# Performance work log

Measured on AMD Instinct MI355X. Metric: run time of the kernel, lower is better.

The kernel has to match this reference:

```python
import jax, jax.numpy as jnp
import numpy as np

B, L, T = 4096, 1024, 32
START, STOP = T - 2, T - 1
NEG = -10000.0


def setup_inputs() -> dict:
    key = jax.random.key(0)
    k1, k2, k3 = jax.random.split(key, 3)
    feats = jax.random.normal(k1, (B, L, T), dtype=jnp.float32)
    transitions = jax.random.normal(k2, (T, T), dtype=jnp.float32)
    # CRF structural constraints from __init__: nothing transitions TO START,
    # nothing transitions FROM STOP. transitions[next, prev] convention.
    transitions = transitions.at[START, :].set(NEG).at[:, STOP].set(NEG)
    tags = jax.random.randint(k3, (B, L), 0, T - 2, dtype=jnp.int64)
    return {"feats": feats, "transitions": transitions, "tags": tags}


def reference(feats, transitions, tags):
    # feats: [B, L, T] emissions, transitions: [T, T] (next, prev), tags: [B, L]
    b, l, t = feats.shape

    # ---- forward algorithm (log partition), scan over time ----
    init = jnp.full((b, t), NEG, dtype=feats.dtype).at[:, START].set(0.0)

    def step(fv, feat_t):  # fv: [B, T] over prev tags, feat_t: [B, T]
        # tag_var[b, next, prev] = fv[b, prev] + trans[next, prev] + emit[b, next]
        tag_var = fv[:, None, :] + transitions[None, :, :] + feat_t[:, :, None]
        return jax.nn.logsumexp(tag_var, axis=2), None

    fv, _ = jax.lax.scan(step, init, jnp.swapaxes(feats, 0, 1))  # scan over L
    alpha = jax.nn.logsumexp(fv + transitions[STOP][None, :], axis=1)  # [B]

    # ---- gold path score ----
    tags_ext = jnp.concatenate(
        [jnp.full((b, 1), START, dtype=tags.dtype), tags], axis=1
    )  # [B, L+1]
    trans_score = transitions[tags_ext[:, 1:], tags_ext[:, :-1]].sum(axis=1)
    emit_score = jnp.take_along_axis(feats, tags[:, :, None], axis=2)[:, :, 0].sum(axis=1)
    gold = trans_score + emit_score + transitions[STOP, tags[:, -1]]

    return alpha - gold  # per-sequence negative log-likelihood [B]
```

## Files before the change

### kernel.cpp

```cpp
#include <hip/hip_runtime.h>
#include <hip/hip_bf16.h>


#define BATCH 4096
#define LSEQ  1024
#define T     32
#define START 30
#define STOP  31

typedef __attribute__((ext_vector_type(8))) short short8;
typedef __attribute__((ext_vector_type(4))) float f32x4;

static __device__ __forceinline__ short bf16b(float x) {
    union { __hip_bfloat16 h; short s; } u;
    u.h = __float2bfloat16(x);
    return u.s;
}

__global__ __launch_bounds__(64) void crf_fwd_mfma(
    const float* __restrict__ feats,
    const float* __restrict__ trans,
    const int*   __restrict__ tags,
    float*       __restrict__ out)
{
    __shared__ float trans_s[T * T];
    const int lane = threadIdx.x;
    for (int i = lane; i < T * T; i += 64) trans_s[i] = trans[i];
    __syncthreads();

    const int n = lane & 15;
    const int q = lane >> 4;
    const int b = blockIdx.x * 16 + n;

    short8 a1, a2;
    {
        const int s1 = 8 * (n >> 2) + (n & 3);
        const int s2 = s1 + 4;
#pragma unroll
        for (int j = 0; j < 8; ++j) {
            a1[j] = bf16b(__expf(trans_s[s1 * T + 8 * q + j]));
            a2[j] = bf16b(__expf(trans_s[s2 * T + 8 * q + j]));
        }
    }

    short8 bfrag;
#pragma unroll
    for (int j = 0; j < 8; ++j) bfrag[j] = 0;
    if (q == 3) bfrag[6] = bf16b(1.0f);

    const f32x4* fp = (const f32x4*)(feats + (size_t)b * (LSEQ * T) + 8 * q);
    const int*   tb = tags + (size_t)b * LSEQ;

    f32x4 fr0[8], fr1[8];
    int   tbuf[8];
#pragma unroll
    for (int i = 0; i < 8; ++i) {
        fr0[i] = fp[i * 8];
        fr1[i] = fp[i * 8 + 1];
        tbuf[i] = tb[i];
    }

    float mAcc  = 0.0f;
    float mAccF = 0.0f;
    float gold_trans = 0.0f;
    float gold_emit  = 0.0f;
    int   prev_tag = START;
    float ev[8];

    const f32x4 zacc = {0.f, 0.f, 0.f, 0.f};

#define CRF_STEP(l, slot, DO_PF)                                               \
    {                                                                          \
        const f32x4 f0  = fr0[slot];                                           \
        const f32x4 f1  = fr1[slot];                                           \
        const int   tag = tbuf[slot];                                          \
        if (DO_PF) {                                                           \
            fr0[slot]  = fp[((l) + 8) * 8];                                    \
            fr1[slot]  = fp[((l) + 8) * 8 + 1];                                \
            tbuf[slot] = tb[(l) + 8];                                          \
        }                                                                      \
                      \
        const float f00 = __shfl(f0[0], n, 64);                                \
        float e0[4], e1[4];                                                    \
        _Pragma("unroll")                                                      \
        for (int r = 0; r < 4; ++r) {                                          \
            e0[r] = __expf(f0[r] - f00);                                       \
            e1[r] = __expf(f1[r] - f00);                                       \
        }                                                                      \
        f32x4 c1 = __builtin_amdgcn_mfma_f32_16x16x32_bf16(a1, bfrag, zacc, 0, 0, 0); \
        f32x4 c2 = __builtin_amdgcn_mfma_f32_16x16x32_bf16(a2, bfrag, zacc, 0, 0, 0); \
                             \
        const float cb  = __shfl(c1[0], n, 64);   \
        const float inv = __builtin_amdgcn_rcpf(cb);                           \
        mAcc  += __logf(cb);            \
        mAccF += f00;                                                          \
        _Pragma("unroll")                                                      \
        for (int r = 0; r < 4; ++r) {                                          \
            ev[r]     = (c1[r] * e0[r]) * inv;                                 \
            ev[4 + r] = (c2[r] * e1[r]) * inv;                                 \
        }                                                                      \
        _Pragma("unroll")                                                      \
        for (int j = 0; j < 8; ++j) bfrag[j] = bf16b(ev[j]);                   \
         \
        gold_trans += trans_s[tag * T + prev_tag];                             \
        {                                                                      \
            const f32x4 fs  = (tag & 4) ? f1 : f0;                             \
            const float p01 = (tag & 1) ? fs[1] : fs[0];                       \
            const float p23 = (tag & 1) ? fs[3] : fs[2];                       \
            const float pk  = (tag & 2) ? p23 : p01;                           \
            if ((tag >> 3) == q) gold_emit += pk;                              \
        }                                                                      \
        prev_tag = tag;                                                        \
    }

    for (int lo = 0; lo < LSEQ - 8; lo += 8) {
#pragma unroll
        for (int i = 0; i < 8; ++i) CRF_STEP(lo + i, i, 1)
    }
#pragma unroll
    for (int i = 0; i < 8; ++i) CRF_STEP(LSEQ - 8 + i, i, 0)
#undef CRF_STEP

    float s = 0.0f;
#pragma unroll
    for (int j = 0; j < 8; ++j)
        s += ev[j] * __expf(trans_s[STOP * T + 8 * q + j]);
    s += __shfl_xor(s, 16, 64);
    s += __shfl_xor(s, 32, 64);
    const float alpha = mAcc + mAccF + __logf(s);

    float ge = gold_emit;
    ge += __shfl_xor(ge, 16, 64);
    ge += __shfl_xor(ge, 32, 64);
    const float gold = ge + gold_trans + trans_s[STOP * T + prev_tag];

    if (lane < 16) out[b] = alpha - gold;
}

extern "C" void kernel_launch(void* const* d_in, const int* in_sizes, int n_in,
                              void* d_out, int out_size, void* d_ws, size_t ws_size,
                              hipStream_t stream) {
    const float* feats = (const float*)d_in[0];
    const float* trans = (const float*)d_in[1];
    const int*   tags  = (const int*)d_in[2];
    float*       out   = (float*)d_out;

    crf_fwd_mfma<<<BATCH / 16, 64, 0, stream>>>(feats, trans, tags, out);
}
```

Baseline: 787.8 us.

## Defer renormalization to every 8 steps and precompute next-step emission exps

Drops the per-step max-shift (shuffle, reciprocal, log) in favour of a fixed ln(64) offset on the emissions, and renormalizes the forward vector only once every 8 steps. The next step's exponentials are computed ahead, off the MFMA-dependent critical path. This shortens the serial dependency chain of each recurrence step. The risk is overflow or underflow in the bf16 and fp32 forward vector between renormalizations, because there is no per-step max shift.

```diff
diff --git a/kernel.cpp b/kernel.cpp
--- a/kernel.cpp
+++ b/kernel.cpp
@@ -7,6 +7,9 @@
 #define T     32
 #define START 30
 #define STOP  31
+
+#define LN64 4.158883083f
+#define SUM_LN64 4258.6963f
 
 typedef __attribute__((ext_vector_type(8))) short short8;
 typedef __attribute__((ext_vector_type(4))) float f32x4;
@@ -60,16 +63,26 @@
         tbuf[i] = tb[i];
     }
 
-    float mAcc  = 0.0f;
-    float mAccF = 0.0f;
+    float mAcc = 0.0f;
     float gold_trans = 0.0f;
     float gold_emit  = 0.0f;
     int   prev_tag = START;
     float ev[8];
+    float eCur[8];
+
+    {
+        const f32x4 g0 = fr0[0];
+        const f32x4 g1 = fr1[0];
+#pragma unroll
+        for (int r = 0; r < 4; ++r) {
+            eCur[r]     = __expf(g0[r] - LN64);
+            eCur[4 + r] = __expf(g1[r] - LN64);
+        }
+    }
 
     const f32x4 zacc = {0.f, 0.f, 0.f, 0.f};
 
-#define CRF_STEP(l, slot, DO_PF)                                               \
+#define CRF_STEP(l, slot, DO_PF, DO_NEXT, DO_RENORM)                           \
     {                                                                          \
         const f32x4 f0  = fr0[slot];                                           \
         const f32x4 f1  = fr1[slot];                                           \
@@ -79,25 +92,12 @@
             fr1[slot]  = fp[((l) + 8) * 8 + 1];                                \
             tbuf[slot] = tb[(l) + 8];                                          \
         }                                                                      \
-                      \
-        const float f00 = __shfl(f0[0], n, 64);                                \
-        float e0[4], e1[4];                                                    \
+        f32x4 c1 = __builtin_amdgcn_mfma_f32_16x16x32_bf16(a1, bfrag, zacc, 0, 0, 0); \
+        f32x4 c2 = __builtin_amdgcn_mfma_f32_16x16x32_bf16(a2, bfrag, zacc, 0, 0, 0); \
         _Pragma("unroll")                                                      \
         for (int r = 0; r < 4; ++r) {                                          \
-            e0[r] = __expf(f0[r] - f00);                                       \
-            e1[r] = __expf(f1[r] - f00);                                       \
-        }                                                                      \
-        f32x4 c1 = __builtin_amdgcn_mfma_f32_16x16x32_bf16(a1, bfrag, zacc, 0, 0, 0); \
-        f32x4 c2 = __builtin_amdgcn_mfma_f32_16x16x32_bf16(a2, bfrag, zacc, 0, 0, 0); \
-                             \
-        const float cb  = __shfl(c1[0], n, 64);   \
-        const float inv = __builtin_amdgcn_rcpf(cb);                           \
-        mAcc  += __logf(cb);            \
-        mAccF += f00;                                                          \
-        _Pragma("unroll")                                                      \
-        for (int r = 0; r < 4; ++r) {                                          \
-            ev[r]     = (c1[r] * e0[r]) * inv;                                 \
-            ev[4 + r] = (c2[r] * e1[r]) * inv;                                 \
+            ev[r]     = c1[r] * eCur[r];                                       \
+            ev[4 + r] = c2[r] * eCur[4 + r];                                   \
         }                                                                      \
         _Pragma("unroll")                                                      \
         for (int j = 0; j < 8; ++j) bfrag[j] = bf16b(ev[j]);                   \
@@ -111,14 +111,43 @@
             if ((tag >> 3) == q) gold_emit += pk;                              \
         }                                                                      \
         prev_tag = tag;                                                        \
+        if (DO_NEXT) {  \
+            const int   ns = ((slot) + 1) & 7;                                 \
+            const f32x4 g0 = fr0[ns];                                          \
+            const f32x4 g1 = fr1[ns];                                          \
+            _Pragma("unroll")                                                  \
+            for (int r = 0; r < 4; ++r) {                                      \
+                eCur[r]     = __expf(g0[r] - LN64);                            \
+                eCur[4 + r] = __expf(g1[r] - LN64);                            \
+            }                                                                  \
+        }                                                                      \
+        if (DO_RENORM) {          \
+            const float cb = __shfl(c1[0], n, 64);       \
+            const float iv = __builtin_amdgcn_rcpf(cb);                        \
+            mAcc += __logf(cb);                                                \
+            _Pragma("unroll")                                                  \
+            for (int j = 0; j < 8; ++j) eCur[j] *= iv;                         \
+        }                                                                      \
     }
 
     for (int lo = 0; lo < LSEQ - 8; lo += 8) {
-#pragma unroll
-        for (int i = 0; i < 8; ++i) CRF_STEP(lo + i, i, 1)
+        CRF_STEP(lo + 0, 0, 1, 1, 0)
+        CRF_STEP(lo + 1, 1, 1, 1, 0)
+        CRF_STEP(lo + 2, 2, 1, 1, 0)
+        CRF_STEP(lo + 3, 3, 1, 1, 0)
+        CRF_STEP(lo + 4, 4, 1, 1, 0)
+        CRF_STEP(lo + 5, 5, 1, 1, 0)
+        CRF_STEP(lo + 6, 6, 1, 1, 0)
+        CRF_STEP(lo + 7, 7, 1, 1, 1)
     }
-#pragma unroll
-    for (int i = 0; i < 8; ++i) CRF_STEP(LSEQ - 8 + i, i, 0)
+    CRF_STEP(LSEQ - 8, 0, 0, 1, 0)
+    CRF_STEP(LSEQ - 7, 1, 0, 1, 0)
+    CRF_STEP(LSEQ - 6, 2, 0, 1, 0)
+    CRF_STEP(LSEQ - 5, 3, 0, 1, 0)
+    CRF_STEP(LSEQ - 4, 4, 0, 1, 0)
+    CRF_STEP(LSEQ - 3, 5, 0, 1, 0)
+    CRF_STEP(LSEQ - 2, 6, 0, 1, 0)
+    CRF_STEP(LSEQ - 1, 7, 0, 0, 0)
 #undef CRF_STEP
 
     float s = 0.0f;
@@ -127,7 +156,7 @@
         s += ev[j] * __expf(trans_s[STOP * T + 8 * q + j]);
     s += __shfl_xor(s, 16, 64);
     s += __shfl_xor(s, 32, 64);
-    const float alpha = mAcc + mAccF + __logf(s);
+    const float alpha = mAcc + SUM_LN64 + __logf(s);
 
     float ge = gold_emit;
     ge += __shfl_xor(ge, 16, 64);
```

After: 789.9 us. Within noise of the previous version (+0.3%).
